# Optimization experiments

Hardware: AMD Instinct MI355X
Metric: run time of the kernel (lower is better)

## Reference

```python
import jax, jax.numpy as jnp
import numpy as np

B = 32768
MARGIN = 0.1
P = 2.0          # norm_degree
EPS_BN = 1e-3    # BatchNorm1d eps=0.001
EPS_PD = 1e-6    # F.pairwise_distance eps


def setup_inputs() -> dict:
    key = jax.random.key(0)
    ks = jax.random.split(key, 40)
    W = lambda k, o, i: jax.random.normal(k, (o, i), jnp.float32) * 0.01
    inp = {
        'img_p': jax.random.normal(ks[0], (B, 300), jnp.float32),
        'img_n': jax.random.normal(ks[1], (B, 300), jnp.float32),
        'tag':   jax.random.normal(ks[2], (B, 300), jnp.float32),
        'lat':   jax.random.uniform(ks[3], (B, 1), jnp.float32),
        'lon':   jax.random.uniform(ks[4], (B, 1), jnp.float32),
        # fc_i_1 (Linear 300->1024 + BN)
        'Wi1': W(ks[5], 1024, 300), 'bi1': jnp.zeros(1024), 'gi1': jnp.ones(1024), 'bti1': jnp.zeros(1024),
        # fc_i_2, fc_i_3
        'Wi2': W(ks[6], 1024, 1024), 'bi2': jnp.zeros(1024),
        'Wi3': W(ks[7], 300, 1024), 'bi3': jnp.zeros(300),
        # fc_loc (Linear 2->10 + BN)
        'Wloc': W(ks[8], 10, 2), 'bloc': jnp.zeros(10), 'gloc': jnp.ones(10), 'btloc': jnp.zeros(10),
        # fc_mm_1..3 (Linear + BN), fc_mm_4
        'Wm1': W(ks[9], 1024, 310), 'bm1': jnp.zeros(1024), 'gm1': jnp.ones(1024), 'btm1': jnp.zeros(1024),
        'Wm2': W(ks[10], 1024, 1024), 'bm2': jnp.zeros(1024), 'gm2': jnp.ones(1024), 'btm2': jnp.zeros(1024),
        'Wm3': W(ks[11], 1024, 1024), 'bm3': jnp.zeros(1024), 'gm3': jnp.ones(1024), 'btm3': jnp.zeros(1024),
        'Wm4': W(ks[12], 300, 1024), 'bm4': jnp.zeros(300),
    }
    return inp


def _fc_bn_relu(x, W, b, g, beta):
    # Linear -> BatchNorm1d (training mode, biased batch stats) -> ReLU
    y = x @ W.T + b
    m = jnp.mean(y, axis=0)
    v = jnp.mean((y - m) ** 2, axis=0)
    return jax.nn.relu((y - m) * jax.lax.rsqrt(v + EPS_BN) * g + beta)


def _pairwise_distance(x, y):
    # torch F.pairwise_distance with eps=1e-6
    return jnp.sum(jnp.abs(x - y + EPS_PD) ** P, axis=1) ** (1.0 / P)


def reference(img_p, img_n, tag, lat, lon,
              Wi1, bi1, gi1, bti1, Wi2, bi2, Wi3, bi3,
              Wloc, bloc, gloc, btloc,
              Wm1, bm1, gm1, btm1, Wm2, bm2, gm2, btm2,
              Wm3, bm3, gm3, btm3, Wm4, bm4):
    def img_branch(x):
        x = _fc_bn_relu(x, Wi1, bi1, gi1, bti1)
        x = x @ Wi2.T + bi2
        x = x @ Wi3.T + bi3
        return x
    p = img_branch(img_p)   # [B, 300]
    n = img_branch(img_n)   # [B, 300] (separate BN batch stats, as in torch)
    loc = jnp.concatenate([lat, lon], axis=1)           # [B, 2]
    loc = _fc_bn_relu(loc, Wloc, bloc, gloc, btloc)     # [B, 10]
    a = jnp.concatenate([loc, tag], axis=1)             # [B, 310]
    a = _fc_bn_relu(a, Wm1, bm1, gm1, btm1)
    a = _fc_bn_relu(a, Wm2, bm2, gm2, btm2)
    a = _fc_bn_relu(a, Wm3, bm3, gm3, btm3)
    a = a @ Wm4.T + bm4                                 # [B, 300]
    d_tp = _pairwise_distance(a, p)
    d_tn = _pairwise_distance(a, n)
    # vectorized replacement for the per-element python count loop
    correct = jnp.sum(d_tn - d_tp > MARGIN).astype(jnp.int32).reshape(1)
    return (p, n, a, correct)
```

## Files before the change

### kernel.cpp

```cpp
#include <hip/hip_runtime.h>

typedef _Float16 f16;
typedef _Float16 half8 __attribute__((ext_vector_type(8)));
typedef float f32x4 __attribute__((ext_vector_type(4)));

__device__ __forceinline__ void gl_lds16(const void* g, void* l) {
  __builtin_amdgcn_global_load_lds(
      (__attribute__((address_space(1))) void*)(size_t)g,
      (__attribute__((address_space(3))) void*)l, 16, 0, 0);
}

template <int EPI, int BNA>
__global__ __launch_bounds__(512, 2) void gemm256_k(
    const f16* __restrict__ A, int Ksteps, int KP,
    void* __restrict__ outp, int ldOut, int Ncols,
    float2* __restrict__ partial, int r1, int kz, int oz,
    const f16* __restrict__ B0, const float* __restrict__ bias0,
    const f16* __restrict__ sc0, const f16* __restrict__ sh0,
    const f16* __restrict__ B1, const float* __restrict__ bias1,
    const f16* __restrict__ sc1, const f16* __restrict__ sh1) {
  __shared__ char smem[135168];

  const int t = threadIdx.x;
  const int lane = t & 63;
  const int wave = t >> 6;
  const int wm = wave >> 2, wn = wave & 3;
  const int l16 = lane & 15, lg = lane >> 4;

  int bx = blockIdx.x, by = blockIdx.y;
  {
    const int nwg = gridDim.x * gridDim.y;
    const int wg = bx + gridDim.x * by;
    const int cpx = nwg >> 3;
    const int newid = (wg & 7) * cpx + (wg >> 3);
    bx = newid % gridDim.x;
    by = newid / gridDim.x;
  }
  const int m0 = by * 256;
  const int n0 = bx * 256;

  const f16* Bw = (by >= r1) ? B1 : B0;
  const float* bias = (by >= r1) ? bias1 : bias0;
  const f16* scH = (by >= r1) ? sc1 : sc0;
  const f16* shH = (by >= r1) ? sh1 : sh0;
  const f16* Az = A + (size_t)blockIdx.z * kz;
  Bw += (size_t)blockIdx.z * kz;

  f32x4 acc[8][4] = {};

  const int rA = t >> 3;
  const int g16 = ((t & 7) ^ (rA & 7)) * 16;
  const size_t rstep = (size_t)64 * KP * 2;
  const char* gA = (const char*)Az + (size_t)(m0 + rA) * KP * 2 + g16;
  const char* gB = (const char*)Bw + (size_t)(n0 + rA) * KP * 2 + g16;

  auto stage = [&](int buf, int kt) {
    const char* pA = gA + (size_t)kt * 128;
    const char* pB = gB + (size_t)kt * 128;
    char* d = smem + buf * 65536 + t * 16;
#pragma unroll
    for (int r = 0; r < 4; ++r) {
      gl_lds16(pA + r * rstep, d + r * 8192);
      gl_lds16(pB + r * rstep, d + 32768 + r * 8192);
    }
  };

  if constexpr (BNA) {
    if (t < 128)
      gl_lds16((const char*)scH + t * 16, smem + 131072 + t * 16);
    else if (t < 256)
      gl_lds16((const char*)shH + (t - 128) * 16, smem + 133120 + (t - 128) * 16);
  }
  stage(0, 0);

  const int xA0 = (wm * 128 + l16) * 128;
  const int xB0 = (wn * 64 + l16) * 128;
  const int x8 = l16 & 7;

  for (int kt = 0; kt < Ksteps; ++kt) {
    const int cur = kt & 1;
    if (kt + 1 < Ksteps) {
      stage(cur ^ 1, kt + 1);
      asm volatile("s_waitcnt vmcnt(8)" ::: "memory");
    } else {
      asm volatile("s_waitcnt vmcnt(0)" ::: "memory");
    }
    __builtin_amdgcn_s_barrier();
    asm volatile("" ::: "memory");

    const char* bufA = smem + cur * 65536;
    const char* bufB = bufA + 32768;
#pragma unroll
    for (int kk = 0; kk < 2; ++kk) {
      const int ks = kk * 4 + lg;
      const int oA = xA0 + ((ks ^ x8) << 4);
      const int oB = xB0 + ((ks ^ x8) << 4);
      half8 af[8], bf[4];
#pragma unroll
      for (int m = 0; m < 8; ++m) af[m] = *(const half8*)(bufA + oA + m * 2048);
#pragma unroll
      for (int n = 0; n < 4; ++n) bf[n] = *(const half8*)(bufB + oB + n * 2048);
      if constexpr (BNA) {
        const half8 scv = *(const half8*)(smem + 131072 + kt * 128 + kk * 64 + lg * 16);
        const half8 shv = *(const half8*)(smem + 133120 + kt * 128 + kk * 64 + lg * 16);
        const half8 zeroh = {};
#pragma unroll
        for (int m = 0; m < 8; ++m)
          af[m] = __builtin_elementwise_max((half8)(af[m] * scv + shv), zeroh);
      }
      __builtin_amdgcn_s_setprio(1);
#pragma unroll
      for (int m = 0; m < 8; ++m)
#pragma unroll
        for (int n = 0; n < 4; ++n)
          acc[m][n] = __builtin_amdgcn_mfma_f32_16x16x32_f16(af[m], bf[n], acc[m][n], 0, 0, 0);
      __builtin_amdgcn_s_setprio(0);
    }
    asm volatile("" ::: "memory");
    __builtin_amdgcn_s_barrier();
    asm volatile("" ::: "memory");
  }

  __syncthreads();

  float* const swv = (float*)smem + wave * 1152;
  float biasv[4];
#pragma unroll
  for (int n = 0; n < 4; ++n) {
    const int c = n0 + wn * 64 + n * 16 + l16;
    biasv[n] = (bias != nullptr && c < Ncols) ? bias[c] : 0.f;
  }
  float cs[4] = {}, cq[4] = {};
  const int rowr = lane >> 2;
  const int colc = (lane & 3) << 4;

#pragma unroll
  for (int m = 0; m < 8; ++m) {
#pragma unroll
    for (int n = 0; n < 4; ++n)
#pragma unroll
      for (int r = 0; r < 4; ++r) {
        const float v = acc[m][n][r] + biasv[n];
        swv[(lg * 4 + r) * 68 + n * 16 + l16] = v;
        if constexpr (EPI == 0) {
          cs[n] += v;
          cq[n] += v * v;
        }
      }
    asm volatile("s_waitcnt lgkmcnt(0)" ::: "memory");
    const float* sp = swv + rowr * 68 + colc;
    const int grow = m0 + wm * 128 + m * 16 + rowr;
    if constexpr (EPI == 2) {
      float* rp = (float*)outp + (size_t)blockIdx.z * oz + (size_t)grow * ldOut;
#pragma unroll
      for (int j = 0; j < 4; ++j) {
        const int c = n0 + wn * 64 + colc + j * 4;
        const f32x4 v = *(const f32x4*)(sp + j * 4);
        if (c + 3 < Ncols) {
          *(f32x4*)(rp + c) = v;
        } else {
#pragma unroll
          for (int e = 0; e < 4; ++e)
            if (c + e < Ncols) rp[c + e] = v[e];
        }
      }
    } else {
      f16* dp = (f16*)outp + (size_t)grow * ldOut + n0 + wn * 64 + colc;
      half8 h0, h1;
#pragma unroll
      for (int e = 0; e < 4; ++e) {
        h0[e] = (f16)sp[e];
        h0[4 + e] = (f16)sp[4 + e];
        h1[e] = (f16)sp[8 + e];
        h1[4 + e] = (f16)sp[12 + e];
      }
      *(half8*)dp = h0;
      *(half8*)(dp + 8) = h1;
    }
    asm volatile("s_waitcnt lgkmcnt(0)" ::: "memory");
  }

  if constexpr (EPI == 0) {
    float2* pp = partial + ((size_t)(by * 2 + wm) * 4 + lg) * 1024 + n0 + wn * 64 + l16;
#pragma unroll
    for (int n = 0; n < 4; ++n) pp[n * 16] = make_float2(cs[n], cq[n]);
  }
}

__global__ void bn_red_k(const float2* __restrict__ partial, float2* __restrict__ part2) {
  const int c = blockIdx.x * 256 + threadIdx.x;
  const int chunk = blockIdx.y;
  const float2* p = partial + (size_t)chunk * 64 * 1024 + c;
  float s = 0.f, q = 0.f;
#pragma unroll 4
  for (int i = 0; i < 64; ++i) {
    float2 v = p[(size_t)i * 1024];
    s += v.x;
    q += v.y;
  }
  part2[(size_t)chunk * 1024 + c] = make_float2(s, q);
}

__global__ void bn_fin_k(const float2* __restrict__ part2, int chunkStart, int nchunks,
                         const float* __restrict__ g, const float* __restrict__ beta,
                         f16* __restrict__ scH, f16* __restrict__ shH, float invB) {
  const int c = blockIdx.x * 256 + threadIdx.x;
  float s = 0.f, q = 0.f;
  const float2* p = part2 + (size_t)chunkStart * 1024 + c;
  for (int i = 0; i < nchunks; ++i) {
    float2 v = p[(size_t)i * 1024];
    s += v.x;
    q += v.y;
  }
  float m = s * invB;
  float var = q * invB - m * m;
  float sc = rsqrtf(var + 1e-3f) * g[c];
  scH[c] = (f16)sc;
  shH[c] = (f16)(beta[c] - m * sc);
}

__global__ void bn_fin3_k(const float2* __restrict__ part2, int cps, float invB,
                          const float* __restrict__ g0, const float* __restrict__ b0,
                          f16* __restrict__ so0, f16* __restrict__ sh0,
                          const float* __restrict__ g1, const float* __restrict__ b1,
                          f16* __restrict__ so1, f16* __restrict__ sh1,
                          const float* __restrict__ g2, const float* __restrict__ b2,
                          f16* __restrict__ so2, f16* __restrict__ sh2) {
  const int j = blockIdx.y;
  const float* g = j == 0 ? g0 : (j == 1 ? g1 : g2);
  const float* bt = j == 0 ? b0 : (j == 1 ? b1 : b2);
  f16* so = j == 0 ? so0 : (j == 1 ? so1 : so2);
  f16* sh = j == 0 ? sh0 : (j == 1 ? sh1 : sh2);
  const int c = blockIdx.x * 256 + threadIdx.x;
  float s = 0.f, q = 0.f;
  const float2* p = part2 + (size_t)j * cps * 1024 + c;
  for (int i = 0; i < cps; ++i) {
    float2 v = p[(size_t)i * 1024];
    s += v.x;
    q += v.y;
  }
  float m = s * invB;
  float var = q * invB - m * m;
  float sc = rsqrtf(var + 1e-3f) * g[c];
  so[c] = (f16)sc;
  sh[c] = (f16)(bt[c] - m * sc);
}

__global__ void cvt_all_k(const float* __restrict__ Wi1, const float* __restrict__ Wm1,
                          const float* __restrict__ Wi3, const float* __restrict__ Wm2,
                          const float* __restrict__ Wm3, const float* __restrict__ Wm4,
                          f16* __restrict__ Wi1p, f16* __restrict__ Wm1p,
                          f16* __restrict__ Wi3p, f16* __restrict__ Wm2p,
                          f16* __restrict__ Wm3p, f16* __restrict__ Wm4p) {
  const int k = blockIdx.x * 256 + threadIdx.x;
  const int row = blockIdx.y;
  const float* src;
  f16* dst;
  int n, K, KP, Nreal;
  if (row < 2048) {
    KP = 384;
    if (row < 1024) { src = Wi1; dst = Wi1p; n = row; K = 300; Nreal = 1024; }
    else { src = Wm1; dst = Wm1p; n = row - 1024; K = 310; Nreal = 1024; }
  } else {
    KP = 1024;
    if (row < 2560) { src = Wi3; dst = Wi3p; n = row - 2048; K = 1024; Nreal = 300; }
    else if (row < 3584) { src = Wm2; dst = Wm2p; n = row - 2560; K = 1024; Nreal = 1024; }
    else if (row < 4608) { src = Wm3; dst = Wm3p; n = row - 3584; K = 1024; Nreal = 1024; }
    else { src = Wm4; dst = Wm4p; n = row - 4608; K = 1024; Nreal = 300; }
  }
  if (k >= KP) return;
  float v = (n < Nreal && k < K) ? src[(size_t)n * K + k] : 0.f;
  dst[(size_t)n * KP + k] = (f16)v;
}

__global__ void cvt_wT_k(const float* __restrict__ W, f16* __restrict__ Wt) {
  __shared__ f16 tile[64][65];
  const int bx = blockIdx.x * 64, by = blockIdx.y * 64;
  const int tc = threadIdx.x & 63, tr = threadIdx.x >> 6;
#pragma unroll
  for (int r = tr; r < 64; r += 4)
    tile[r][tc] = (f16)W[(size_t)(by + r) * 1024 + bx + tc];
  __syncthreads();
#pragma unroll
  for (int r = tr; r < 64; r += 4)
    Wt[(size_t)(bx + r) * 1024 + by + tc] = tile[tc][r];
}

__global__ void cvt_in_k(const float* __restrict__ ip, const float* __restrict__ in_,
                         const float* __restrict__ tg, f16* __restrict__ Ain, int B) {
  const int gid = blockIdx.x * 256 + threadIdx.x;
  const int row = gid / 48;
  const int c0 = (gid - row * 48) * 8;
  if (row >= B) return;
  half8 vp = {}, vn = {}, vm = {};
  const float* rp = ip + (size_t)row * 300;
  const float* rn = in_ + (size_t)row * 300;
  const float* rt = tg + (size_t)row * 300;
#pragma unroll
  for (int e = 0; e < 8; ++e) {
    const int c = c0 + e;
    if (c < 300) {
      vp[e] = (f16)rp[c];
      vn[e] = (f16)rn[c];
    }
    if (c >= 10 && c < 310) vm[e] = (f16)rt[c - 10];
  }
  const size_t o = (size_t)row * 384 + c0;
  *(half8*)(Ain + o) = vp;
  *(half8*)(Ain + (size_t)B * 384 + o) = vn;
  *(half8*)(Ain + (size_t)2 * B * 384 + o) = vm;
}

__global__ void fold_red_k(const float* __restrict__ pf, f16* __restrict__ Wf) {
  const int i = blockIdx.x * 256 + threadIdx.x;
  float s = 0.f;
#pragma unroll
  for (int z = 0; z < 8; ++z) s += pf[(size_t)z * 524288 + i];
  Wf[i] = (f16)s;
}

__global__ void bfold_k(const f16* __restrict__ Wi3p, const float* __restrict__ bi2,
                        const float* __restrict__ bi3, float* __restrict__ bf) {
  const int n = blockIdx.x;
  const int t = threadIdx.x;
  float s = 0.f;
  for (int j = t; j < 1024; j += 256) s += (float)Wi3p[(size_t)n * 1024 + j] * bi2[j];
#pragma unroll
  for (int off = 32; off; off >>= 1) s += __shfl_xor(s, off);
  __shared__ float red[4];
  if ((t & 63) == 0) red[t >> 6] = s;
  __syncthreads();
  if (t == 0) bf[n] = red[0] + red[1] + red[2] + red[3] + (n < 300 ? bi3[n] : 0.f);
}

__global__ void loc_stats_k(const float* __restrict__ lat, const float* __restrict__ lon,
                            const float* __restrict__ Wloc, const float* __restrict__ bloc,
                            float* __restrict__ partial) {
  const int t = threadIdx.x;
  const int row = blockIdx.x * 256 + t;
  float la = lat[row], lo = lon[row];
  float s[10], q[10];
#pragma unroll
  for (int j = 0; j < 10; ++j) {
    float y = la * Wloc[j * 2] + lo * Wloc[j * 2 + 1] + bloc[j];
    s[j] = y;
    q[j] = y * y;
  }
#pragma unroll
  for (int j = 0; j < 10; ++j)
    for (int off = 32; off; off >>= 1) {
      s[j] += __shfl_xor(s[j], off);
      q[j] += __shfl_xor(q[j], off);
    }
  __shared__ float red[4][20];
  const int wave = t >> 6, lane = t & 63;
  if (lane == 0) {
#pragma unroll
    for (int j = 0; j < 10; ++j) {
      red[wave][j] = s[j];
      red[wave][10 + j] = q[j];
    }
  }
  __syncthreads();
  if (t < 20) partial[blockIdx.x * 20 + t] = red[0][t] + red[1][t] + red[2][t] + red[3][t];
}

__global__ void loc_fin_k(const float* __restrict__ partial, int nblk,
                          const float* __restrict__ g, const float* __restrict__ beta,
                          float2* __restrict__ ss, float invB) {
  int t = threadIdx.x;
  if (t < 10) {
    float s = 0.f, q = 0.f;
    for (int b = 0; b < nblk; ++b) {
      s += partial[b * 20 + t];
      q += partial[b * 20 + 10 + t];
    }
    float m = s * invB;
    float var = q * invB - m * m;
    float sc = rsqrtf(var + 1e-3f) * g[t];
    ss[t] = make_float2(sc, beta[t] - m * sc);
  }
}

__global__ void loc_write_k(const float* __restrict__ lat, const float* __restrict__ lon,
                            const float* __restrict__ Wloc, const float* __restrict__ bloc,
                            const float2* __restrict__ ss, f16* __restrict__ Am) {
  const int row = blockIdx.x * 256 + threadIdx.x;
  float la = lat[row], lo = lon[row];
  f16* dst = Am + (size_t)row * 384;
#pragma unroll
  for (int j = 0; j < 10; ++j) {
    float y = la * Wloc[j * 2] + lo * Wloc[j * 2 + 1] + bloc[j];
    float2 sv = ss[j];
    dst[j] = (f16)fmaxf(y * sv.x + sv.y, 0.f);
  }
}

__global__ void count_k(const float* __restrict__ P, const float* __restrict__ Nn,
                        const float* __restrict__ Aa, int B, int* __restrict__ cnt) {
  const int gw = (blockIdx.x * blockDim.x + threadIdx.x) >> 6;
  const int lane = threadIdx.x & 63;
  const int nw = (gridDim.x * blockDim.x) >> 6;
  int local = 0;
  for (int row = gw; row < B; row += nw) {
    const float* ar = Aa + (size_t)row * 300;
    const float* pr = P + (size_t)row * 300;
    const float* nr = Nn + (size_t)row * 300;
    float sp = 0.f, sn = 0.f;
    for (int e = lane; e < 300; e += 64) {
      float av = ar[e];
      float d1 = av - pr[e] + 1e-6f;
      float d2 = av - nr[e] + 1e-6f;
      sp += d1 * d1;
      sn += d2 * d2;
    }
#pragma unroll
    for (int off = 32; off; off >>= 1) {
      sp += __shfl_xor(sp, off);
      sn += __shfl_xor(sn, off);
    }
    if (lane == 0 && (sqrtf(sn) - sqrtf(sp) > 0.1f)) ++local;
  }
  if (lane == 0 && local) atomicAdd(cnt, local);
}

__global__ void zero_i32(int* p) {
  if (threadIdx.x == 0 && blockIdx.x == 0) *p = 0;
}
__global__ void write_cnt_k(const int* c, float* o) {
  if (threadIdx.x == 0 && blockIdx.x == 0) *o = (float)(*c);
}

extern "C" void kernel_launch(void* const* d_in, const int* in_sizes, int n_in,
                              void* d_out, int out_size, void* d_ws, size_t ws_size,
                              hipStream_t stream) {
  const float* img_p = (const float*)d_in[0];
  const float* img_n = (const float*)d_in[1];
  const float* tag = (const float*)d_in[2];
  const float* lat = (const float*)d_in[3];
  const float* lon = (const float*)d_in[4];
  const float* Wi1 = (const float*)d_in[5];
  const float* bi1 = (const float*)d_in[6];
  const float* gi1 = (const float*)d_in[7];
  const float* bti1 = (const float*)d_in[8];
  const float* Wi2 = (const float*)d_in[9];
  const float* bi2 = (const float*)d_in[10];
  const float* Wi3 = (const float*)d_in[11];
  const float* bi3 = (const float*)d_in[12];
  const float* Wloc = (const float*)d_in[13];
  const float* bloc = (const float*)d_in[14];
  const float* gloc = (const float*)d_in[15];
  const float* btloc = (const float*)d_in[16];
  const float* Wm1 = (const float*)d_in[17];
  const float* bm1 = (const float*)d_in[18];
  const float* gm1 = (const float*)d_in[19];
  const float* btm1 = (const float*)d_in[20];
  const float* Wm2 = (const float*)d_in[21];
  const float* bm2 = (const float*)d_in[22];
  const float* gm2 = (const float*)d_in[23];
  const float* btm2 = (const float*)d_in[24];
  const float* Wm3 = (const float*)d_in[25];
  const float* bm3 = (const float*)d_in[26];
  const float* gm3 = (const float*)d_in[27];
  const float* btm3 = (const float*)d_in[28];
  const float* Wm4 = (const float*)d_in[29];
  const float* bm4 = (const float*)d_in[30];

  const int B = in_sizes[3];
  const int MT = B / 256;
  float* out = (float*)d_out;
  float* outP = out;
  float* outN = out + (size_t)B * 300;
  float* outA = out + (size_t)2 * B * 300;
  float* outC = out + (size_t)3 * B * 300;

  char* w = (char*)d_ws;
  auto alloc = [&](size_t bytes) {
    char* p = w;
    w += (bytes + 255) & ~(size_t)255;
    return p;
  };

  f16* Wi1p = (f16*)alloc((size_t)1024 * 384 * 2);
  f16* Wm1p = (f16*)alloc((size_t)1024 * 384 * 2);
  f16* Wi2T = (f16*)alloc((size_t)1024 * 1024 * 2);
  f16* Wi3p = (f16*)alloc((size_t)512 * 1024 * 2);
  f16* Wm2p = (f16*)alloc((size_t)1024 * 1024 * 2);
  f16* Wm3p = (f16*)alloc((size_t)1024 * 1024 * 2);
  f16* Wm4p = (f16*)alloc((size_t)512 * 1024 * 2);
  f16* Wfold = (f16*)alloc((size_t)512 * 1024 * 2);
  float* bfold = (float*)alloc(512 * 4);
  f16* ssT = (f16*)alloc(10 * 1024 * 2);
  f16 *scP1 = ssT, *shP1 = ssT + 1024, *scN1 = ssT + 2048, *shN1 = ssT + 3072;
  f16 *scM1 = ssT + 4096, *shM1 = ssT + 5120, *scM2 = ssT + 6144, *shM2 = ssT + 7168;
  f16 *scM3 = ssT + 8192, *shM3 = ssT + 9216;
  float* locpart = (float*)alloc((size_t)(B / 256) * 20 * 4);
  float2* locss = (float2*)alloc(16 * 8);
  int* cnt = (int*)alloc(256);
  f16* Ain = (f16*)alloc((size_t)3 * B * 384 * 2);
  f16* Am = Ain + (size_t)2 * B * 384;
  f16* ACT0 = (f16*)alloc((size_t)3 * B * 1024 * 2);
  f16* ACT0m = ACT0 + (size_t)2 * B * 1024;
  f16* ACT1m = (f16*)alloc((size_t)B * 1024 * 2);
  float2* part = (float2*)alloc((size_t)3072 * 1024 * 8);
  float* partF = (float*)part;
  float2* part2 = (float2*)alloc((size_t)48 * 1024 * 8);
  (void)ws_size;
  (void)out_size;
  (void)n_in;

  const float invB = 1.f / (float)B;
  const int BIG = 1 << 30;

  cvt_all_k<<<dim3(4, 5120), 256, 0, stream>>>(Wi1, Wm1, Wi3, Wm2, Wm3, Wm4,
                                               Wi1p, Wm1p, Wi3p, Wm2p, Wm3p, Wm4p);
  cvt_wT_k<<<dim3(16, 16), 256, 0, stream>>>(Wi2, Wi2T);
  cvt_in_k<<<dim3(B * 48 / 256), 256, 0, stream>>>(img_p, img_n, tag, Ain, B);

  loc_stats_k<<<dim3(B / 256), 256, 0, stream>>>(lat, lon, Wloc, bloc, locpart);
  loc_fin_k<<<dim3(1), 64, 0, stream>>>(locpart, B / 256, gloc, btloc, locss, invB);
  loc_write_k<<<dim3(B / 256), 256, 0, stream>>>(lat, lon, Wloc, bloc, locss, Am);

  bfold_k<<<dim3(512), 256, 0, stream>>>(Wi3p, bi2, bi3, bfold);
  gemm256_k<2, 0><<<dim3(4, 2, 8), 512, 0, stream>>>(
      Wi3p, 2, 1024, partF, 1024, 1024, nullptr, BIG, 128, 524288,
      Wi2T, nullptr, nullptr, nullptr, Wi2T, nullptr, nullptr, nullptr);
  fold_red_k<<<dim3(2048), 256, 0, stream>>>(partF, Wfold);

  gemm256_k<0, 0><<<dim3(4, 3 * MT), 512, 0, stream>>>(
      Ain, 6, 384, ACT0, 1024, 1024, part, 2 * MT, 0, 0,
      Wi1p, bi1, nullptr, nullptr, Wm1p, bm1, nullptr, nullptr);
  bn_red_k<<<dim3(4, 48), 256, 0, stream>>>(part, part2);
  bn_fin3_k<<<dim3(4, 3), 256, 0, stream>>>(
      part2, 16, invB,
      gi1, bti1, scP1, shP1, gi1, bti1, scN1, shN1, gm1, btm1, scM1, shM1);

  gemm256_k<2, 1><<<dim3(2, 2 * MT), 512, 0, stream>>>(
      ACT0, 16, 1024, outP, 300, 300, part, MT, 0, 0,
      Wfold, bfold, scP1, shP1, Wfold, bfold, scN1, shN1);

  gemm256_k<0, 1><<<dim3(4, MT), 512, 0, stream>>>(
      ACT0m, 16, 1024, ACT1m, 1024, 1024, part, BIG, 0, 0,
      Wm2p, bm2, scM1, shM1, Wm2p, bm2, scM1, shM1);
  bn_red_k<<<dim3(4, 16), 256, 0, stream>>>(part, part2);
  bn_fin_k<<<dim3(4), 256, 0, stream>>>(part2, 0, 16, gm2, btm2, scM2, shM2, invB);
  gemm256_k<0, 1><<<dim3(4, MT), 512, 0, stream>>>(
      ACT1m, 16, 1024, ACT0, 1024, 1024, part, BIG, 0, 0,
      Wm3p, bm3, scM2, shM2, Wm3p, bm3, scM2, shM2);
  bn_red_k<<<dim3(4, 16), 256, 0, stream>>>(part, part2);
  bn_fin_k<<<dim3(4), 256, 0, stream>>>(part2, 0, 16, gm3, btm3, scM3, shM3, invB);
  gemm256_k<2, 1><<<dim3(2, MT), 512, 0, stream>>>(
      ACT0, 16, 1024, outA, 300, 300, part, BIG, 0, 0,
      Wm4p, bm4, scM3, shM3, Wm4p, bm4, scM3, shM3);

  zero_i32<<<1, 64, 0, stream>>>(cnt);
  count_k<<<dim3(1024), 256, 0, stream>>>(outP, outN, outA, B, cnt);
  write_cnt_k<<<1, 64, 0, stream>>>(cnt, outC);
}
```

Measured before the change: 714.5 us.

## Switch GEMM to 4-stage LDS pipeline with 32-wide K tiles

The GEMM main loop moves from a double-buffered 64-wide K tile to a four-slot ring of 32-wide K tiles, keeping three tiles in flight with graded vmcnt waits. The LDS swizzle and fragment offsets are changed to match, and all launch sites double their K step counts. The goal is to hide global-to-LDS latency better while keeping the same shared-memory footprint. In exchange there are twice as many barriers per K and less MFMA work between syncs. The epilogue also reads LDS as vector f32x4 loads before converting to half.

```diff
diff --git a/kernel.cpp b/kernel.cpp
--- a/kernel.cpp
+++ b/kernel.cpp
@@ -48,21 +48,20 @@
 
   f32x4 acc[8][4] = {};
 
-  const int rA = t >> 3;
-  const int g16 = ((t & 7) ^ (rA & 7)) * 16;
-  const size_t rstep = (size_t)64 * KP * 2;
+  const int rA = t >> 2;
+  const int g16 = ((t & 3) ^ ((t >> 3) & 3)) * 16;
+  const size_t rstep = (size_t)128 * KP * 2;
   const char* gA = (const char*)Az + (size_t)(m0 + rA) * KP * 2 + g16;
   const char* gB = (const char*)Bw + (size_t)(n0 + rA) * KP * 2 + g16;
 
-  auto stage = [&](int buf, int kt) {
-    const char* pA = gA + (size_t)kt * 128;
-    const char* pB = gB + (size_t)kt * 128;
-    char* d = smem + buf * 65536 + t * 16;
-#pragma unroll
-    for (int r = 0; r < 4; ++r) {
-      gl_lds16(pA + r * rstep, d + r * 8192);
-      gl_lds16(pB + r * rstep, d + 32768 + r * 8192);
-    }
+  auto stage = [&](int slot, int kt) {
+    const char* pA = gA + (size_t)kt * 64;
+    const char* pB = gB + (size_t)kt * 64;
+    char* d = smem + slot * 32768 + t * 16;
+    gl_lds16(pA, d);
+    gl_lds16(pA + rstep, d + 8192);
+    gl_lds16(pB, d + 16384);
+    gl_lds16(pB + rstep, d + 24576);
   };
 
   if constexpr (BNA) {
@@ -72,50 +71,49 @@
       gl_lds16((const char*)shH + (t - 128) * 16, smem + 133120 + (t - 128) * 16);
   }
   stage(0, 0);
-
-  const int xA0 = (wm * 128 + l16) * 128;
-  const int xB0 = (wn * 64 + l16) * 128;
-  const int x8 = l16 & 7;
+  if (Ksteps > 1) stage(1, 1);
+  if (Ksteps > 2) stage(2, 2);
+
+  const int xsw = (lg ^ ((l16 >> 1) & 3)) << 4;
+  const int oA0 = (wm * 128 + l16) * 64 + xsw;
+  const int oB0 = (wn * 64 + l16) * 64 + xsw;
 
   for (int kt = 0; kt < Ksteps; ++kt) {
-    const int cur = kt & 1;
-    if (kt + 1 < Ksteps) {
-      stage(cur ^ 1, kt + 1);
+    if (kt + 3 < Ksteps) {
+      stage((kt + 3) & 3, kt + 3);
+      asm volatile("s_waitcnt vmcnt(12)" ::: "memory");
+    } else if (kt + 3 == Ksteps) {
       asm volatile("s_waitcnt vmcnt(8)" ::: "memory");
+    } else if (kt + 2 == Ksteps) {
+      asm volatile("s_waitcnt vmcnt(4)" ::: "memory");
     } else {
       asm volatile("s_waitcnt vmcnt(0)" ::: "memory");
     }
     __builtin_amdgcn_s_barrier();
     asm volatile("" ::: "memory");
 
-    const char* bufA = smem + cur * 65536;
-    const char* bufB = bufA + 32768;
-#pragma unroll
-    for (int kk = 0; kk < 2; ++kk) {
-      const int ks = kk * 4 + lg;
-      const int oA = xA0 + ((ks ^ x8) << 4);
-      const int oB = xB0 + ((ks ^ x8) << 4);
-      half8 af[8], bf[4];
-#pragma unroll
-      for (int m = 0; m < 8; ++m) af[m] = *(const half8*)(bufA + oA + m * 2048);
-#pragma unroll
-      for (int n = 0; n < 4; ++n) bf[n] = *(const half8*)(bufB + oB + n * 2048);
-      if constexpr (BNA) {
-        const half8 scv = *(const half8*)(smem + 131072 + kt * 128 + kk * 64 + lg * 16);
-        const half8 shv = *(const half8*)(smem + 133120 + kt * 128 + kk * 64 + lg * 16);
-        const half8 zeroh = {};
-#pragma unroll
-        for (int m = 0; m < 8; ++m)
-          af[m] = __builtin_elementwise_max((half8)(af[m] * scv + shv), zeroh);
-      }
-      __builtin_amdgcn_s_setprio(1);
+    const char* bufA = smem + (kt & 3) * 32768;
+    const char* bufB = bufA + 16384;
+    half8 af[8], bf[4];
+#pragma unroll
+    for (int m = 0; m < 8; ++m) af[m] = *(const half8*)(bufA + oA0 + m * 1024);
+#pragma unroll
+    for (int n = 0; n < 4; ++n) bf[n] = *(const half8*)(bufB + oB0 + n * 1024);
+    if constexpr (BNA) {
+      const half8 scv = *(const half8*)(smem + 131072 + kt * 64 + lg * 16);
+      const half8 shv = *(const half8*)(smem + 133120 + kt * 64 + lg * 16);
+      const half8 zeroh = {};
 #pragma unroll
       for (int m = 0; m < 8; ++m)
-#pragma unroll
-        for (int n = 0; n < 4; ++n)
-          acc[m][n] = __builtin_amdgcn_mfma_f32_16x16x32_f16(af[m], bf[n], acc[m][n], 0, 0, 0);
-      __builtin_amdgcn_s_setprio(0);
-    }
+        af[m] = __builtin_elementwise_max((half8)(af[m] * scv + shv), zeroh);
+    }
+    __builtin_amdgcn_s_setprio(1);
+#pragma unroll
+    for (int m = 0; m < 8; ++m)
+#pragma unroll
+      for (int n = 0; n < 4; ++n)
+        acc[m][n] = __builtin_amdgcn_mfma_f32_16x16x32_f16(af[m], bf[n], acc[m][n], 0, 0, 0);
+    __builtin_amdgcn_s_setprio(0);
     asm volatile("" ::: "memory");
     __builtin_amdgcn_s_barrier();
     asm volatile("" ::: "memory");
@@ -166,13 +164,17 @@
       }
     } else {
       f16* dp = (f16*)outp + (size_t)grow * ldOut + n0 + wn * 64 + colc;
+      const f32x4 v0 = *(const f32x4*)(sp);
+      const f32x4 v1 = *(const f32x4*)(sp + 4);
+      const f32x4 v2 = *(const f32x4*)(sp + 8);
+      const f32x4 v3 = *(const f32x4*)(sp + 12);
       half8 h0, h1;
 #pragma unroll
       for (int e = 0; e < 4; ++e) {
-        h0[e] = (f16)sp[e];
-        h0[4 + e] = (f16)sp[4 + e];
-        h1[e] = (f16)sp[8 + e];
-        h1[4 + e] = (f16)sp[12 + e];
+        h0[e] = (f16)v0[e];
+        h0[4 + e] = (f16)v1[e];
+        h1[e] = (f16)v2[e];
+        h1[4 + e] = (f16)v3[e];
       }
       *(half8*)dp = h0;
       *(half8*)(dp + 8) = h1;
@@ -523,12 +525,12 @@
 
   bfold_k<<<dim3(512), 256, 0, stream>>>(Wi3p, bi2, bi3, bfold);
   gemm256_k<2, 0><<<dim3(4, 2, 8), 512, 0, stream>>>(
-      Wi3p, 2, 1024, partF, 1024, 1024, nullptr, BIG, 128, 524288,
+      Wi3p, 4, 1024, partF, 1024, 1024, nullptr, BIG, 128, 524288,
       Wi2T, nullptr, nullptr, nullptr, Wi2T, nullptr, nullptr, nullptr);
   fold_red_k<<<dim3(2048), 256, 0, stream>>>(partF, Wfold);
 
   gemm256_k<0, 0><<<dim3(4, 3 * MT), 512, 0, stream>>>(
-      Ain, 6, 384, ACT0, 1024, 1024, part, 2 * MT, 0, 0,
+      Ain, 12, 384, ACT0, 1024, 1024, part, 2 * MT, 0, 0,
       Wi1p, bi1, nullptr, nullptr, Wm1p, bm1, nullptr, nullptr);
   bn_red_k<<<dim3(4, 48), 256, 0, stream>>>(part, part2);
   bn_fin3_k<<<dim3(4, 3), 256, 0, stream>>>(
@@ -536,21 +538,21 @@
       gi1, bti1, scP1, shP1, gi1, bti1, scN1, shN1, gm1, btm1, scM1, shM1);
 
   gemm256_k<2, 1><<<dim3(2, 2 * MT), 512, 0, stream>>>(
-      ACT0, 16, 1024, outP, 300, 300, part, MT, 0, 0,
+      ACT0, 32, 1024, outP, 300, 300, part, MT, 0, 0,
       Wfold, bfold, scP1, shP1, Wfold, bfold, scN1, shN1);
 
   gemm256_k<0, 1><<<dim3(4, MT), 512, 0, stream>>>(
-      ACT0m, 16, 1024, ACT1m, 1024, 1024, part, BIG, 0, 0,
+      ACT0m, 32, 1024, ACT1m, 1024, 1024, part, BIG, 0, 0,
       Wm2p, bm2, scM1, shM1, Wm2p, bm2, scM1, shM1);
   bn_red_k<<<dim3(4, 16), 256, 0, stream>>>(part, part2);
   bn_fin_k<<<dim3(4), 256, 0, stream>>>(part2, 0, 16, gm2, btm2, scM2, shM2, invB);
   gemm256_k<0, 1><<<dim3(4, MT), 512, 0, stream>>>(
-      ACT1m, 16, 1024, ACT0, 1024, 1024, part, BIG, 0, 0,
+      ACT1m, 32, 1024, ACT0, 1024, 1024, part, BIG, 0, 0,
       Wm3p, bm3, scM2, shM2, Wm3p, bm3, scM2, shM2);
   bn_red_k<<<dim3(4, 16), 256, 0, stream>>>(part, part2);
   bn_fin_k<<<dim3(4), 256, 0, stream>>>(part2, 0, 16, gm3, btm3, scM3, shM3, invB);
   gemm256_k<2, 1><<<dim3(2, MT), 512, 0, stream>>>(
-      ACT0, 16, 1024, outA, 300, 300, part, BIG, 0, 0,
+      ACT0, 32, 1024, outA, 300, 300, part, BIG, 0, 0,
       Wm4p, bm4, scM3, shM3, Wm4p, bm4, scM3, shM3);
 
   zero_i32<<<1, 64, 0, stream>>>(cnt);
```

Result: slower. 740.5 us (+3.6%).
